# Performance work log

Hardware: AMD Instinct MI355X
Metric: run time of the kernel (lower is better)

Reference implementation:

```python
import jax, jax.numpy as jnp
import numpy as np

N = 50000
E = 800000
D = 128
EPS = 1e-5


def setup_inputs() -> dict:
    key = jax.random.key(0)
    ks = jax.random.split(key, 12)
    s1 = 1.0 / np.sqrt(2 * D)
    s2 = 1.0 / np.sqrt(D)
    return {
        "x": jax.random.normal(ks[0], (N, D), dtype=jnp.float32),
        "edge_index": jax.random.randint(ks[1], (2, E), 0, N, dtype=jnp.int32),
        # message MLP: Linear(2D->D), SiLU, Linear(D->D)
        "wm1": jax.random.uniform(ks[2], (2 * D, D), jnp.float32, -s1, s1),
        "bm1": jax.random.uniform(ks[3], (D,), jnp.float32, -s1, s1),
        "wm2": jax.random.uniform(ks[4], (D, D), jnp.float32, -s2, s2),
        "bm2": jax.random.uniform(ks[5], (D,), jnp.float32, -s2, s2),
        # update MLP: Linear(2D->D), SiLU, Linear(D->D)
        "wu1": jax.random.uniform(ks[6], (2 * D, D), jnp.float32, -s1, s1),
        "bu1": jax.random.uniform(ks[7], (D,), jnp.float32, -s1, s1),
        "wu2": jax.random.uniform(ks[8], (D, D), jnp.float32, -s2, s2),
        "bu2": jax.random.uniform(ks[9], (D,), jnp.float32, -s2, s2),
        # LayerNorm affine
        "gamma": jnp.ones((D,), jnp.float32),
        "beta": jnp.zeros((D,), jnp.float32),
    }


def reference(x, edge_index, wm1, bm1, wm2, bm2, wu1, bu1, wu2, bu2, gamma, beta):
    row, col = edge_index[0], edge_index[1]
    # gather endpoints and build message input [E, 2D]
    msg_in = jnp.concatenate([x[row], x[col]], axis=-1)
    h = jax.nn.silu(msg_in @ wm1 + bm1)
    messages = h @ wm2 + bm2  # [E, D]
    # scatter-add aggregate into destination rows
    aggr = jax.ops.segment_sum(messages, row, num_segments=x.shape[0])  # [N, D]
    upd_in = jnp.concatenate([x, aggr], axis=-1)  # [N, 2D]
    u = jax.nn.silu(upd_in @ wu1 + bu1)
    out = u @ wu2 + bu2  # [N, D]
    # residual + LayerNorm
    y = x + out
    mu = jnp.mean(y, axis=-1, keepdims=True)
    var = jnp.var(y, axis=-1, keepdims=True)
    yn = (y - mu) * jax.lax.rsqrt(var + EPS)
    return yn * gamma + beta
```

## Files before the change

### kernel.cpp

```cpp
#include <hip/hip_runtime.h>
#include <hip/hip_bf16.h>

#define NN 50000
#define EE 800000
#define DD 128
#define TILES (EE / 64)
#define NB_SCAN ((NN + 255) / 256)

typedef __attribute__((ext_vector_type(8))) short bf8v;
typedef __attribute__((ext_vector_type(4))) float f4v;
typedef __attribute__((ext_vector_type(4))) unsigned int u4v;

static __device__ __forceinline__ unsigned int bpack2(float lo, float hi) {
    union { __hip_bfloat162 h2; unsigned int u; } c;
    c.h2 = __float22bfloat162_rn(float2{lo, hi});
    return c.u;
}
static __device__ __forceinline__ u4v pack8(f4v a, f4v b) {
    u4v r;
    r[0] = bpack2(a[0], a[1]); r[1] = bpack2(a[2], a[3]);
    r[2] = bpack2(b[0], b[1]); r[3] = bpack2(b[2], b[3]);
    return r;
}
static __device__ __forceinline__ short f2bf_s(float f) {
    union { __hip_bfloat16 h; short s; } c;
    c.h = __float2bfloat16(f);
    return c.s;
}
static __device__ __forceinline__ float bf_lo(unsigned int u) {
    union { unsigned int u; float f; } c; c.u = u << 16; return c.f;
}
static __device__ __forceinline__ float bf_hi(unsigned int u) {
    union { unsigned int u; float f; } c; c.u = u & 0xffff0000u; return c.f;
}
static __device__ __forceinline__ float silu(float v) {
    return v * __builtin_amdgcn_rcpf(1.f + __expf(-v));
}

__global__ __launch_bounds__(256) void setup_kernel(
    const float* __restrict__ wm1, const float* __restrict__ wm2,
    const float* __restrict__ wu1, const float* __restrict__ wu2,
    short* __restrict__ out, int* __restrict__ cnt, float* __restrict__ aggr) {
    int idx = blockIdx.x * 256 + threadIdx.x;
    {
        const float* src; int l;
        if      (idx < 32768) { src = wm1; l = idx; }
        else if (idx < 49152) { src = wm2; l = idx - 32768; }
        else if (idx < 81920) { src = wu1; l = idx - 49152; }
        else                  { src = wu2; l = idx - 81920; }
        int e    = l & 7;
        int lane = (l >> 3) & 63;
        int ntg  = (l >> 9) & 7;
        int kc   = l >> 12;
        out[idx] = f2bf_s(src[(kc * 32 + (lane >> 4) * 8 + e) * DD + ntg * 16 + (lane & 15)]);
    }
    for (int i = idx; i < NN; i += 98304) cnt[i] = 0;
    f4v z = (f4v){0.f, 0.f, 0.f, 0.f};
    for (int i = idx; i < NN * DD / 4; i += 98304) ((f4v*)aggr)[i] = z;
}

__global__ __launch_bounds__(256) void hist_rank_kernel(const int* __restrict__ ei,
                                                        int* __restrict__ cnt,
                                                        int* __restrict__ rank) {
    int e = blockIdx.x * 256 + threadIdx.x;
    if (e < EE) rank[e] = atomicAdd(&cnt[ei[e]], 1);
}

__global__ __launch_bounds__(256) void scanA_kernel(const int* __restrict__ cnt,
                                                    int* __restrict__ bsum) {
    __shared__ int sd[256];
    int t = threadIdx.x;
    int i = blockIdx.x * 256 + t;
    sd[t] = (i < NN) ? cnt[i] : 0;
    __syncthreads();
    for (int off = 128; off > 0; off >>= 1) {
        if (t < off) sd[t] += sd[t + off];
        __syncthreads();
    }
    if (t == 0) bsum[blockIdx.x] = sd[0];
}

__global__ __launch_bounds__(256) void scanB_kernel(const int* __restrict__ bsum,
                                                    int* __restrict__ bscan) {
    __shared__ int sd[256];
    int t = threadIdx.x;
    int v = (t < NB_SCAN) ? bsum[t] : 0;
    sd[t] = v;
    __syncthreads();
    for (int off = 1; off < 256; off <<= 1) {
        int u = (t >= off) ? sd[t - off] : 0;
        __syncthreads();
        sd[t] += u;
        __syncthreads();
    }
    if (t < NB_SCAN) bscan[t] = sd[t] - v;
}

__global__ __launch_bounds__(256) void scanC_kernel(const int* __restrict__ cnt,
                                                    const int* __restrict__ bscan,
                                                    int* __restrict__ cursor) {
    __shared__ int sd[256];
    int t = threadIdx.x;
    int i = blockIdx.x * 256 + t;
    int v = (i < NN) ? cnt[i] : 0;
    sd[t] = v;
    __syncthreads();
    for (int off = 1; off < 256; off <<= 1) {
        int u = (t >= off) ? sd[t - off] : 0;
        __syncthreads();
        sd[t] += u;
        __syncthreads();
    }
    if (i < NN) cursor[i] = bscan[blockIdx.x] + sd[t] - v;
}

__global__ __launch_bounds__(256) void rows_fill_kernel(const int* __restrict__ cursor,
                                                        const int* __restrict__ cnt,
                                                        int* __restrict__ rows) {
    int r = blockIdx.x * 256 + threadIdx.x;
    if (r < NN) {
        int b = cursor[r], n = cnt[r];
        for (int i = 0; i < n; ++i) rows[b + i] = r;
    }
}

__global__ __launch_bounds__(256) void scatter_col_rank_kernel(const int* __restrict__ ei,
                                                               const int* __restrict__ cursor,
                                                               const int* __restrict__ rank,
                                                               int* __restrict__ srtc) {
    int e = blockIdx.x * 256 + threadIdx.x;
    if (e < EE) srtc[cursor[ei[e]] + rank[e]] = ei[EE + e];
}

__global__ __launch_bounds__(256) void scatter_col_atomic_kernel(const int* __restrict__ ei,
                                                                 int* __restrict__ cursor,
                                                                 int* __restrict__ srtc) {
    int e = blockIdx.x * 256 + threadIdx.x;
    if (e < EE) {
        int pos = atomicAdd(&cursor[ei[e]], 1);
        srtc[pos] = ei[EE + e];
    }
}

__global__ __launch_bounds__(256) void pq_kernel(
    const float* __restrict__ x,
    const short* __restrict__ W1f, const float* __restrict__ bm1,
    short* __restrict__ P, short* __restrict__ Q)
{
    __shared__ char smem[32768];
    const int tid = threadIdx.x;
    const int w = tid >> 6, lane = tid & 63;
    const int rbase = blockIdx.x * 64;
    const int rloc = tid >> 2, s = tid & 3;

    {
        int rg = rbase + rloc;
        int rgc = rg < NN ? rg : NN - 1;
        const float* xr = x + (size_t)rgc * DD + s * 32;
        int swz = (rloc & 7) << 4;
        #pragma unroll
        for (int j = 0; j < 4; ++j) {
            f4v a0 = *(const f4v*)(xr + j * 8);
            f4v a1 = *(const f4v*)(xr + j * 8 + 4);
            *(u4v*)(smem + ((rloc * 256 + s * 64 + j * 16) ^ swz)) = pack8(a0, a1);
        }
    }

    bf8v w1t[4][2], w1b[4][2];
    #pragma unroll
    for (int kc = 0; kc < 4; ++kc)
        #pragma unroll
        for (int nt = 0; nt < 2; ++nt) {
            w1t[kc][nt] = *(const bf8v*)(W1f + (((kc * 8) + (w * 2 + nt)) * 64 + lane) * 8);
            w1b[kc][nt] = *(const bf8v*)(W1f + ((((kc + 4) * 8) + (w * 2 + nt)) * 64 + lane) * 8);
        }
    __syncthreads();

    f4v accP[4][2], accQ[4][2];
    #pragma unroll
    for (int mt = 0; mt < 4; ++mt)
        #pragma unroll
        for (int nt = 0; nt < 2; ++nt) {
            accP[mt][nt] = (f4v){0.f, 0.f, 0.f, 0.f};
            accQ[mt][nt] = (f4v){0.f, 0.f, 0.f, 0.f};
        }
    #pragma unroll
    for (int kc = 0; kc < 4; ++kc) {
        bf8v a[4];
        int kb = kc * 64 + (lane >> 4) * 16;
        #pragma unroll
        for (int mt = 0; mt < 4; ++mt) {
            int row = mt * 16 + (lane & 15);
            a[mt] = *(const bf8v*)(smem + ((row * 256 + kb) ^ ((row & 7) << 4)));
        }
        #pragma unroll
        for (int mt = 0; mt < 4; ++mt)
            #pragma unroll
            for (int nt = 0; nt < 2; ++nt) {
                accP[mt][nt] = __builtin_amdgcn_mfma_f32_16x16x32_bf16(a[mt], w1t[kc][nt], accP[mt][nt], 0, 0, 0);
                accQ[mt][nt] = __builtin_amdgcn_mfma_f32_16x16x32_bf16(a[mt], w1b[kc][nt], accQ[mt][nt], 0, 0, 0);
            }
    }
    __syncthreads();

    int col0 = w * 32 + (lane & 15);
    float b1a = bm1[col0], b1b = bm1[col0 + 16];
    #pragma unroll
    for (int mt = 0; mt < 4; ++mt)
        #pragma unroll
        for (int nt = 0; nt < 2; ++nt) {
            float bb = nt ? b1b : b1a;
            int col = col0 + nt * 16;
            #pragma unroll
            for (int r = 0; r < 4; ++r) {
                int row = mt * 16 + (lane >> 4) * 4 + r;
                int off = (row * 256 + col * 2) ^ ((row & 7) << 4);
                *(short*)(smem + off)         = f2bf_s(accP[mt][nt][r] + bb);
                *(short*)(smem + 16384 + off) = f2bf_s(accQ[mt][nt][r]);
            }
        }
    __syncthreads();

    {
        int rg = rbase + rloc;
        if (rg < NN) {
            int swz = (rloc & 7) << 4;
            #pragma unroll
            for (int j = 0; j < 4; ++j) {
                int off = (rloc * 256 + s * 64 + j * 16) ^ swz;
                *(u4v*)(P + (size_t)rg * DD + s * 32 + j * 8) = *(const u4v*)(smem + off);
                *(u4v*)(Q + (size_t)rg * DD + s * 32 + j * 8) = *(const u4v*)(smem + 16384 + off);
            }
        }
    }
}

__global__ __launch_bounds__(256, 8) void edge_kernel(
    const short* __restrict__ P, const short* __restrict__ Q,
    const int* __restrict__ rows, const int* __restrict__ srtc,
    const int* __restrict__ ei, int use_sorted,
    const short* __restrict__ W2f, const float* __restrict__ bm2,
    float* __restrict__ aggr)
{
    __shared__ char smem[16384 + 256];
    char* Hs = smem;
    int* rows_s = (int*)(smem + 16384);

    const int tid = threadIdx.x;
    const int w = tid >> 6, lane = tid & 63;
    const int rloc = tid >> 2, s = tid & 3;

    {
        int eg = blockIdx.x * 64 + rloc;
        int r, c;
        if (use_sorted) { r = rows[eg]; c = srtc[eg]; }
        else            { r = ei[eg];   c = ei[EE + eg]; }
        if (s == 0) rows_s[rloc] = r;
        const u4v* pr = (const u4v*)(P + (size_t)r * DD + s * 32);
        const u4v* qr = (const u4v*)(Q + (size_t)c * DD + s * 32);
        int swz = (rloc & 7) << 4;
        #pragma unroll
        for (int j = 0; j < 4; ++j) {
            u4v pj = pr[j], qj = qr[j];
            u4v hv;
            #pragma unroll
            for (int k2 = 0; k2 < 4; ++k2) {
                float lo = silu(bf_lo(pj[k2]) + bf_lo(qj[k2]));
                float hi = silu(bf_hi(pj[k2]) + bf_hi(qj[k2]));
                hv[k2] = bpack2(lo, hi);
            }
            *(u4v*)(Hs + ((rloc * 256 + s * 64 + j * 16) ^ swz)) = hv;
        }
    }

    bf8v w2f[4][2];
    #pragma unroll
    for (int kc = 0; kc < 4; ++kc)
        #pragma unroll
        for (int nt = 0; nt < 2; ++nt)
            w2f[kc][nt] = *(const bf8v*)(W2f + (((kc * 8) + (w * 2 + nt)) * 64 + lane) * 8);
    int col0 = w * 32 + (lane & 15);
    float b2a = bm2[col0], b2b = bm2[col0 + 16];

    __syncthreads();

    f4v acc2[4][2];
    #pragma unroll
    for (int mt = 0; mt < 4; ++mt)
        #pragma unroll
        for (int nt = 0; nt < 2; ++nt)
            acc2[mt][nt] = (f4v){0.f, 0.f, 0.f, 0.f};
    #pragma unroll
    for (int kc = 0; kc < 4; ++kc) {
        bf8v a[4];
        int kb = kc * 64 + (lane >> 4) * 16;
        #pragma unroll
        for (int mt = 0; mt < 4; ++mt) {
            int row = mt * 16 + (lane & 15);
            a[mt] = *(const bf8v*)(Hs + ((row * 256 + kb) ^ ((row & 7) << 4)));
        }
        #pragma unroll
        for (int mt = 0; mt < 4; ++mt)
            #pragma unroll
            for (int nt = 0; nt < 2; ++nt)
                acc2[mt][nt] = __builtin_amdgcn_mfma_f32_16x16x32_bf16(a[mt], w2f[kc][nt], acc2[mt][nt], 0, 0, 0);
    }
    __syncthreads();

    #pragma unroll
    for (int mt = 0; mt < 4; ++mt)
        #pragma unroll
        for (int nt = 0; nt < 2; ++nt) {
            int col = col0 + nt * 16;
            float bb = nt ? b2b : b2a;
            #pragma unroll
            for (int r = 0; r < 4; ++r) {
                int row = mt * 16 + (lane >> 4) * 4 + r;
                *(short*)(Hs + ((row * 256 + col * 2) ^ ((row & 7) << 4))) = f2bf_s(acc2[mt][nt][r] + bb);
            }
        }
    __syncthreads();

    {
        int col = tid & 127;
        int r0 = (tid >> 7) * 32;
        int cur = rows_s[r0];
        float run = 0.f;
        for (int k = 0; k < 32; ++k) {
            int row = r0 + k;
            int d = rows_s[row];
            unsigned short sv = *(const unsigned short*)(Hs + ((row * 256 + col * 2) ^ ((row & 7) << 4)));
            union { unsigned int u; float f; } c; c.u = ((unsigned int)sv) << 16;
            if (d != cur) {
                unsafeAtomicAdd(aggr + (size_t)cur * DD + col, run);
                run = 0.f; cur = d;
            }
            run += c.f;
        }
        unsafeAtomicAdd(aggr + (size_t)cur * DD + col, run);
    }
}

__global__ __launch_bounds__(256, 4) void node_kernel(
    const float* __restrict__ x, const float* __restrict__ aggr,
    const short* __restrict__ U1f, const short* __restrict__ U2f,
    const float* __restrict__ bu1, const float* __restrict__ bu2,
    const float* __restrict__ gmm, const float* __restrict__ bta,
    float* __restrict__ out)
{
    __shared__ char smem[64 * 512 + 2048];
    char* As = smem;
    float* ps  = (float*)(smem + 64 * 512);
    float* ps2 = ps + 256;

    const int tid = threadIdx.x;
    const int w = tid >> 6, lane = tid & 63;
    const int rbase = blockIdx.x * 64;

    {
        int rloc = tid >> 2, s = tid & 3;
        int rg = rbase + rloc;
        int rgc = rg < NN ? rg : 0;
        const float* xr = x + (size_t)rgc * DD + s * 32;
        const float* ar = aggr + (size_t)rgc * DD + s * 32;
        int swz = (rloc & 7) << 4;
        #pragma unroll
        for (int i2 = 0; i2 < 4; ++i2) {
            f4v a0 = *(const f4v*)(xr + i2 * 8);
            f4v a1 = *(const f4v*)(xr + i2 * 8 + 4);
            int addr = rloc * 512 + s * 64 + i2 * 16;
            *(u4v*)(As + (addr ^ swz)) = pack8(a0, a1);
            f4v b0 = *(const f4v*)(ar + i2 * 8);
            f4v b1 = *(const f4v*)(ar + i2 * 8 + 4);
            int addr2 = rloc * 512 + 256 + s * 64 + i2 * 16;
            *(u4v*)(As + (addr2 ^ swz)) = pack8(b0, b1);
        }
    }

    bf8v u1f[8][2], u2f[4][2];
    #pragma unroll
    for (int kc = 0; kc < 8; ++kc)
        #pragma unroll
        for (int nt = 0; nt < 2; ++nt)
            u1f[kc][nt] = *(const bf8v*)(U1f + (((kc * 8) + (w * 2 + nt)) * 64 + lane) * 8);
    #pragma unroll
    for (int kc = 0; kc < 4; ++kc)
        #pragma unroll
        for (int nt = 0; nt < 2; ++nt)
            u2f[kc][nt] = *(const bf8v*)(U2f + (((kc * 8) + (w * 2 + nt)) * 64 + lane) * 8);

    __syncthreads();

    f4v acc[4][2];
    #pragma unroll
    for (int mt = 0; mt < 4; ++mt)
        #pragma unroll
        for (int nt = 0; nt < 2; ++nt)
            acc[mt][nt] = (f4v){0.f, 0.f, 0.f, 0.f};
    #pragma unroll
    for (int kc = 0; kc < 8; ++kc) {
        bf8v a[4];
        int kb = kc * 64 + (lane >> 4) * 16;
        #pragma unroll
        for (int mt = 0; mt < 4; ++mt) {
            int row = mt * 16 + (lane & 15);
            a[mt] = *(const bf8v*)(As + ((row * 512 + kb) ^ ((row & 7) << 4)));
        }
        #pragma unroll
        for (int mt = 0; mt < 4; ++mt)
            #pragma unroll
            for (int nt = 0; nt < 2; ++nt)
                acc[mt][nt] = __builtin_amdgcn_mfma_f32_16x16x32_bf16(a[mt], u1f[kc][nt], acc[mt][nt], 0, 0, 0);
    }
    __syncthreads();

    int col0 = w * 32 + (lane & 15);
    float b1a = bu1[col0], b1b = bu1[col0 + 16];
    #pragma unroll
    for (int mt = 0; mt < 4; ++mt)
        #pragma unroll
        for (int nt = 0; nt < 2; ++nt) {
            float bb = nt ? b1b : b1a;
            int col = col0 + nt * 16;
            #pragma unroll
            for (int r = 0; r < 4; ++r) {
                float v = silu(acc[mt][nt][r] + bb);
                int row = mt * 16 + (lane >> 4) * 4 + r;
                *(short*)(As + ((row * 256 + col * 2) ^ ((row & 7) << 4))) = f2bf_s(v);
            }
        }
    __syncthreads();

    f4v acc2[4][2];
    #pragma unroll
    for (int mt = 0; mt < 4; ++mt)
        #pragma unroll
        for (int nt = 0; nt < 2; ++nt)
            acc2[mt][nt] = (f4v){0.f, 0.f, 0.f, 0.f};
    #pragma unroll
    for (int kc = 0; kc < 4; ++kc) {
        bf8v a[4];
        int kb = kc * 64 + (lane >> 4) * 16;
        #pragma unroll
        for (int mt = 0; mt < 4; ++mt) {
            int row = mt * 16 + (lane & 15);
            a[mt] = *(const bf8v*)(As + ((row * 256 + kb) ^ ((row & 7) << 4)));
        }
        #pragma unroll
        for (int mt = 0; mt < 4; ++mt)
            #pragma unroll
            for (int nt = 0; nt < 2; ++nt)
                acc2[mt][nt] = __builtin_amdgcn_mfma_f32_16x16x32_bf16(a[mt], u2f[kc][nt], acc2[mt][nt], 0, 0, 0);
    }
    __syncthreads();

    float b2a = bu2[col0], b2b = bu2[col0 + 16];
    #pragma unroll
    for (int mt = 0; mt < 4; ++mt)
        #pragma unroll
        for (int nt = 0; nt < 2; ++nt) {
            int col = col0 + nt * 16;
            float bb = nt ? b2b : b2a;
            #pragma unroll
            for (int r = 0; r < 4; ++r) {
                int rowl = mt * 16 + (lane >> 4) * 4 + r;
                int rg = rbase + rowl;
                int rgc = rg < NN ? rg : 0;
                float xv = x[(size_t)rgc * DD + col];
                float y = acc2[mt][nt][r] + bb + xv;
                *(float*)(As + ((rowl * 512 + col * 4) ^ ((rowl & 7) << 4))) = y;
            }
        }
    __syncthreads();

    {
        int rloc = tid >> 2, q = tid & 3;
        float s1 = 0.f, s2 = 0.f;
        #pragma unroll
        for (int i = 0; i < 8; ++i) {
            f4v v = *(const f4v*)(As + ((rloc * 512 + q * 128 + i * 16) ^ ((rloc & 7) << 4)));
            s1 += v[0] + v[1] + v[2] + v[3];
            s2 += v[0] * v[0] + v[1] * v[1] + v[2] * v[2] + v[3] * v[3];
        }
        ps[rloc * 4 + q] = s1;
        ps2[rloc * 4 + q] = s2;
    }
    __syncthreads();
    {
        int rloc = tid >> 2, q = tid & 3;
        float fs  = ps[rloc * 4] + ps[rloc * 4 + 1] + ps[rloc * 4 + 2] + ps[rloc * 4 + 3];
        float fs2 = ps2[rloc * 4] + ps2[rloc * 4 + 1] + ps2[rloc * 4 + 2] + ps2[rloc * 4 + 3];
        float mu  = fs * (1.f / 128.f);
        float var = fs2 * (1.f / 128.f) - mu * mu;
        float inv = rsqrtf(var + 1e-5f);
        int rg = rbase + rloc;
        if (rg < NN) {
            #pragma unroll
            for (int i = 0; i < 8; ++i) {
                int col = q * 32 + i * 4;
                f4v v  = *(const f4v*)(As + ((rloc * 512 + col * 4) ^ ((rloc & 7) << 4)));
                f4v gg = *(const f4v*)(gmm + col);
                f4v bb = *(const f4v*)(bta + col);
                f4v o;
                #pragma unroll
                for (int j = 0; j < 4; ++j)
                    o[j] = (v[j] - mu) * inv * gg[j] + bb[j];
                *(f4v*)(out + (size_t)rg * DD + col) = o;
            }
        }
    }
}

extern "C" void kernel_launch(void* const* d_in, const int* in_sizes, int n_in,
                              void* d_out, int out_size, void* d_ws, size_t ws_size,
                              hipStream_t stream) {
    const float* x    = (const float*)d_in[0];
    const int*   ei   = (const int*)d_in[1];
    const float* wm1  = (const float*)d_in[2];
    const float* bm1  = (const float*)d_in[3];
    const float* wm2  = (const float*)d_in[4];
    const float* bm2  = (const float*)d_in[5];
    const float* wu1  = (const float*)d_in[6];
    const float* bu1  = (const float*)d_in[7];
    const float* wu2  = (const float*)d_in[8];
    const float* bu2  = (const float*)d_in[9];
    const float* gmm  = (const float*)d_in[10];
    const float* bta  = (const float*)d_in[11];
    float* out = (float*)d_out;

    const size_t off_P     = 0;
    const size_t off_Q     = 12800000;
    const size_t off_frags = 25600000;
    const size_t off_cnt   = 25796608;
    const size_t off_cur   = 25996608;
    const size_t off_bsum  = 26196608;
    const size_t off_bscan = 26197632;
    const size_t off_rows  = 26198656;
    const size_t off_srtc  = 29398656;
    const size_t off_rank  = 32598656;
    const size_t need_rank   = 35798656;
    const size_t need_atomic = 32598656;

    char* wsB = (char*)d_ws;
    short* P    = (short*)(wsB + off_P);
    short* Q    = (short*)(wsB + off_Q);
    short* Wf   = (short*)(wsB + off_frags);
    short* W1f  = Wf;
    short* W2f  = Wf + 32768;
    short* U1f  = Wf + 49152;
    short* U2f  = Wf + 81920;
    int*   cnt    = (int*)(wsB + off_cnt);
    int*   cursor = (int*)(wsB + off_cur);
    int*   bsum   = (int*)(wsB + off_bsum);
    int*   bscan  = (int*)(wsB + off_bscan);
    int*   rows   = (int*)(wsB + off_rows);
    int*   srtc   = (int*)(wsB + off_srtc);
    int*   rank   = (int*)(wsB + off_rank);

    float* aggr = (float*)d_out;

    int tier = (ws_size >= need_rank) ? 2 : (ws_size >= need_atomic ? 1 : 0);

    setup_kernel<<<384, 256, 0, stream>>>(wm1, wm2, wu1, wu2, Wf, cnt, aggr);
    pq_kernel<<<(NN + 63) / 64, 256, 0, stream>>>(x, W1f, bm1, P, Q);

    int use_sorted = 0;
    if (tier > 0) {
        hist_rank_kernel<<<(EE + 255) / 256, 256, 0, stream>>>(ei, cnt,
            tier == 2 ? rank : srtc );
        scanA_kernel<<<NB_SCAN, 256, 0, stream>>>(cnt, bsum);
        scanB_kernel<<<1, 256, 0, stream>>>(bsum, bscan);
        scanC_kernel<<<NB_SCAN, 256, 0, stream>>>(cnt, bscan, cursor);
        rows_fill_kernel<<<NB_SCAN, 256, 0, stream>>>(cursor, cnt, rows);
        if (tier == 2)
            scatter_col_rank_kernel<<<(EE + 255) / 256, 256, 0, stream>>>(ei, cursor, rank, srtc);
        else
            scatter_col_atomic_kernel<<<(EE + 255) / 256, 256, 0, stream>>>(ei, cursor, srtc);
        use_sorted = 1;
    }

    edge_kernel<<<TILES, 256, 0, stream>>>(P, Q, rows, srtc, ei, use_sorted, W2f, bm2, aggr);
    node_kernel<<<(NN + 63) / 64, 256, 0, stream>>>(x, aggr, U1f, U2f, bu1, bu2, gmm, bta, out);
}
```

Baseline: 198.1 us.

## Simplify edge sort, fuse rows fill into scan, pair-wise segmented atomics, vectorize residual

Drops the rank-based scatter path and always uses the atomic-cursor scatter, which removes the rank array writes and reads. The rows fill loop is folded into scanC, saving one launch. The edge kernel's segmented reduction now uses 128 threads, each handling two columns with a 32-bit LDS read and two atomics, halving the threads doing reduction work. The node kernel adds the residual x through vectorized f4 loads while computing the LayerNorm statistics, replacing scalar strided loads. The atomic scatter makes the edge order within each segment nondeterministic, and using fewer threads for the reduction may lengthen its critical path.

```diff
diff --git a/kernel.cpp b/kernel.cpp
--- a/kernel.cpp
+++ b/kernel.cpp
@@ -59,11 +59,10 @@
     for (int i = idx; i < NN * DD / 4; i += 98304) ((f4v*)aggr)[i] = z;
 }
 
-__global__ __launch_bounds__(256) void hist_rank_kernel(const int* __restrict__ ei,
-                                                        int* __restrict__ cnt,
-                                                        int* __restrict__ rank) {
+__global__ __launch_bounds__(256) void hist_kernel(const int* __restrict__ ei,
+                                                   int* __restrict__ cnt) {
     int e = blockIdx.x * 256 + threadIdx.x;
-    if (e < EE) rank[e] = atomicAdd(&cnt[ei[e]], 1);
+    if (e < EE) atomicAdd(&cnt[ei[e]], 1);
 }
 
 __global__ __launch_bounds__(256) void scanA_kernel(const int* __restrict__ cnt,
@@ -98,7 +97,8 @@
 
 __global__ __launch_bounds__(256) void scanC_kernel(const int* __restrict__ cnt,
                                                     const int* __restrict__ bscan,
-                                                    int* __restrict__ cursor) {
+                                                    int* __restrict__ cursor,
+                                                    int* __restrict__ rows) {
     __shared__ int sd[256];
     int t = threadIdx.x;
     int i = blockIdx.x * 256 + t;
@@ -111,25 +111,11 @@
         sd[t] += u;
         __syncthreads();
     }
-    if (i < NN) cursor[i] = bscan[blockIdx.x] + sd[t] - v;
-}
-
-__global__ __launch_bounds__(256) void rows_fill_kernel(const int* __restrict__ cursor,
-                                                        const int* __restrict__ cnt,
-                                                        int* __restrict__ rows) {
-    int r = blockIdx.x * 256 + threadIdx.x;
-    if (r < NN) {
-        int b = cursor[r], n = cnt[r];
-        for (int i = 0; i < n; ++i) rows[b + i] = r;
-    }
-}
-
-__global__ __launch_bounds__(256) void scatter_col_rank_kernel(const int* __restrict__ ei,
-                                                               const int* __restrict__ cursor,
-                                                               const int* __restrict__ rank,
-                                                               int* __restrict__ srtc) {
-    int e = blockIdx.x * 256 + threadIdx.x;
-    if (e < EE) srtc[cursor[ei[e]] + rank[e]] = ei[EE + e];
+    if (i < NN) {
+        int c0 = bscan[blockIdx.x] + sd[t] - v;
+        cursor[i] = c0;
+        for (int k = 0; k < v; ++k) rows[c0 + k] = i;
+    }
 }
 
 __global__ __launch_bounds__(256) void scatter_col_atomic_kernel(const int* __restrict__ ei,
@@ -321,23 +307,28 @@
         }
     __syncthreads();
 
-    {
-        int col = tid & 127;
-        int r0 = (tid >> 7) * 32;
+    if (tid < 128) {
+        int pp = tid & 63;
+        int hh = tid >> 6;
+        int cbyte = pp * 4;
+        int r0 = hh * 32;
         int cur = rows_s[r0];
-        float run = 0.f;
+        float run0 = 0.f, run1 = 0.f;
+        #pragma unroll 4
         for (int k = 0; k < 32; ++k) {
             int row = r0 + k;
             int d = rows_s[row];
-            unsigned short sv = *(const unsigned short*)(Hs + ((row * 256 + col * 2) ^ ((row & 7) << 4)));
-            union { unsigned int u; float f; } c; c.u = ((unsigned int)sv) << 16;
+            unsigned int uv = *(const unsigned int*)(Hs + ((row * 256 + cbyte) ^ ((row & 7) << 4)));
             if (d != cur) {
-                unsafeAtomicAdd(aggr + (size_t)cur * DD + col, run);
-                run = 0.f; cur = d;
-            }
-            run += c.f;
-        }
-        unsafeAtomicAdd(aggr + (size_t)cur * DD + col, run);
+                unsafeAtomicAdd(aggr + (size_t)cur * DD + pp * 2,     run0);
+                unsafeAtomicAdd(aggr + (size_t)cur * DD + pp * 2 + 1, run1);
+                run0 = 0.f; run1 = 0.f; cur = d;
+            }
+            run0 += bf_lo(uv);
+            run1 += bf_hi(uv);
+        }
+        unsafeAtomicAdd(aggr + (size_t)cur * DD + pp * 2,     run0);
+        unsafeAtomicAdd(aggr + (size_t)cur * DD + pp * 2 + 1, run1);
     }
 }
 
@@ -356,9 +347,9 @@
     const int tid = threadIdx.x;
     const int w = tid >> 6, lane = tid & 63;
     const int rbase = blockIdx.x * 64;
-
-    {
-        int rloc = tid >> 2, s = tid & 3;
+    const int rloc = tid >> 2, s = tid & 3;
+
+    {
         int rg = rbase + rloc;
         int rgc = rg < NN ? rg : 0;
         const float* xr = x + (size_t)rgc * DD + s * 32;
@@ -464,30 +455,35 @@
             #pragma unroll
             for (int r = 0; r < 4; ++r) {
                 int rowl = mt * 16 + (lane >> 4) * 4 + r;
-                int rg = rbase + rowl;
-                int rgc = rg < NN ? rg : 0;
-                float xv = x[(size_t)rgc * DD + col];
-                float y = acc2[mt][nt][r] + bb + xv;
-                *(float*)(As + ((rowl * 512 + col * 4) ^ ((rowl & 7) << 4))) = y;
-            }
-        }
-    __syncthreads();
-
-    {
-        int rloc = tid >> 2, q = tid & 3;
+                *(float*)(As + ((rowl * 512 + col * 4) ^ ((rowl & 7) << 4))) = acc2[mt][nt][r] + bb;
+            }
+        }
+    __syncthreads();
+
+    {
+        int rg = rbase + rloc;
+        int rgc = rg < NN ? rg : 0;
+        const f4v* xr = (const f4v*)(x + (size_t)rgc * DD + s * 32);
         float s1 = 0.f, s2 = 0.f;
         #pragma unroll
         for (int i = 0; i < 8; ++i) {
-            f4v v = *(const f4v*)(As + ((rloc * 512 + q * 128 + i * 16) ^ ((rloc & 7) << 4)));
-            s1 += v[0] + v[1] + v[2] + v[3];
-            s2 += v[0] * v[0] + v[1] * v[1] + v[2] * v[2] + v[3] * v[3];
-        }
-        ps[rloc * 4 + q] = s1;
-        ps2[rloc * 4 + q] = s2;
-    }
-    __syncthreads();
-    {
-        int rloc = tid >> 2, q = tid & 3;
+            int off = (rloc * 512 + s * 128 + i * 16) ^ ((rloc & 7) << 4);
+            f4v v = *(const f4v*)(As + off);
+            f4v xv = xr[i];
+            f4v y;
+            #pragma unroll
+            for (int j = 0; j < 4; ++j) {
+                y[j] = v[j] + xv[j];
+                s1 += y[j];
+                s2 += y[j] * y[j];
+            }
+            *(f4v*)(As + off) = y;
+        }
+        ps[rloc * 4 + s] = s1;
+        ps2[rloc * 4 + s] = s2;
+    }
+    __syncthreads();
+    {
         float fs  = ps[rloc * 4] + ps[rloc * 4 + 1] + ps[rloc * 4 + 2] + ps[rloc * 4 + 3];
         float fs2 = ps2[rloc * 4] + ps2[rloc * 4 + 1] + ps2[rloc * 4 + 2] + ps2[rloc * 4 + 3];
         float mu  = fs * (1.f / 128.f);
@@ -497,7 +493,7 @@
         if (rg < NN) {
             #pragma unroll
             for (int i = 0; i < 8; ++i) {
-                int col = q * 32 + i * 4;
+                int col = s * 32 + i * 4;
                 f4v v  = *(const f4v*)(As + ((rloc * 512 + col * 4) ^ ((rloc & 7) << 4)));
                 f4v gg = *(const f4v*)(gmm + col);
                 f4v bb = *(const f4v*)(bta + col);
@@ -537,9 +533,7 @@
     const size_t off_bscan = 26197632;
     const size_t off_rows  = 26198656;
     const size_t off_srtc  = 29398656;
-    const size_t off_rank  = 32598656;
-    const size_t need_rank   = 35798656;
-    const size_t need_atomic = 32598656;
+    const size_t need_sort = 32598656;
 
     char* wsB = (char*)d_ws;
     short* P    = (short*)(wsB + off_P);
@@ -555,27 +549,19 @@
     int*   bscan  = (int*)(wsB + off_bscan);
     int*   rows   = (int*)(wsB + off_rows);
     int*   srtc   = (int*)(wsB + off_srtc);
-    int*   rank   = (int*)(wsB + off_rank);
 
     float* aggr = (float*)d_out;
-
-    int tier = (ws_size >= need_rank) ? 2 : (ws_size >= need_atomic ? 1 : 0);
 
     setup_kernel<<<384, 256, 0, stream>>>(wm1, wm2, wu1, wu2, Wf, cnt, aggr);
     pq_kernel<<<(NN + 63) / 64, 256, 0, stream>>>(x, W1f, bm1, P, Q);
 
     int use_sorted = 0;
-    if (tier > 0) {
-        hist_rank_kernel<<<(EE + 255) / 256, 256, 0, stream>>>(ei, cnt,
-            tier == 2 ? rank : srtc );
+    if (ws_size >= need_sort) {
+        hist_kernel<<<(EE + 255) / 256, 256, 0, stream>>>(ei, cnt);
         scanA_kernel<<<NB_SCAN, 256, 0, stream>>>(cnt, bsum);
         scanB_kernel<<<1, 256, 0, stream>>>(bsum, bscan);
-        scanC_kernel<<<NB_SCAN, 256, 0, stream>>>(cnt, bscan, cursor);
-        rows_fill_kernel<<<NB_SCAN, 256, 0, stream>>>(cursor, cnt, rows);
-        if (tier == 2)
-            scatter_col_rank_kernel<<<(EE + 255) / 256, 256, 0, stream>>>(ei, cursor, rank, srtc);
-        else
-            scatter_col_atomic_kernel<<<(EE + 255) / 256, 256, 0, stream>>>(ei, cursor, srtc);
+        scanC_kernel<<<NB_SCAN, 256, 0, stream>>>(cnt, bscan, cursor, rows);
+        scatter_col_atomic_kernel<<<(EE + 255) / 256, 256, 0, stream>>>(ei, cursor, srtc);
         use_sorted = 1;
     }
 
```

Result: slower. 262.1 us (+32.3%).
